# Optimization experiments

Hardware: AMD Instinct MI355X
Metric: run time of the kernel (lower is better)

Reference implementation:

```python
import jax, jax.numpy as jnp
import numpy as np

EPS = 1e-5
CHUNK = 512


def _bn(x, gamma, beta):
    # BatchNorm1d in training mode: biased batch statistics over the batch dim
    m = x.mean(axis=0)
    v = ((x - m) ** 2).mean(axis=0)
    return (x - m) * jax.lax.rsqrt(v + EPS) * gamma + beta


def _xavier(k, fan_in, fan_out):
    lim = float(np.sqrt(6.0 / (fan_in + fan_out)))
    return jax.random.uniform(k, (fan_in, fan_out), minval=-lim, maxval=lim, dtype=jnp.float32)


def setup_inputs() -> dict:
    key = jax.random.key(0)
    ks = jax.random.split(key, 10)
    B, CH_S, CH_H, T = 8192, 512, 2048, 3
    D = CH_H * T  # 6144 = 12 chunks of 512
    inp = {
        "fs": jax.random.normal(ks[0], (B, CH_S), dtype=jnp.float32),
        "ft0": jax.random.normal(ks[1], (B, CH_H), dtype=jnp.float32),
        "ft1": jax.random.normal(ks[2], (B, CH_H), dtype=jnp.float32),
        "ft2": jax.random.normal(ks[3], (B, CH_H), dtype=jnp.float32),
        # fixed (non-trainable in the original: plain tensor) score key [512, 1]
        "score_key": jax.random.uniform(ks[4], (CHUNK, 1), dtype=jnp.float32),
        # align_t: Linear(D,2048) -> BN -> Linear(2048,2048) -> BN -> Linear(2048,CH_H) -> ReLU
        "W1": _xavier(ks[5], D, 2048), "b1": jnp.zeros((2048,), jnp.float32),
        "g1": jnp.ones((2048,), jnp.float32), "beta1": jnp.zeros((2048,), jnp.float32),
        "W2": _xavier(ks[6], 2048, 2048), "b2": jnp.zeros((2048,), jnp.float32),
        "g2": jnp.ones((2048,), jnp.float32), "beta2": jnp.zeros((2048,), jnp.float32),
        "W3": _xavier(ks[7], 2048, CH_H), "b3": jnp.zeros((CH_H,), jnp.float32),
        # extend: Linear(CH_H, D) -> ReLU
        "We": _xavier(ks[8], CH_H, D), "bE": jnp.zeros((D,), jnp.float32),
    }
    return inp


def reference(fs, ft0, ft1, ft2, score_key, W1, b1, g1, beta1, W2, b2, g2, beta2, W3, b3, We, bE):
    # fs is accepted but unused, mirroring the original forward
    ft_all = jnp.concatenate([ft0, ft1, ft2], axis=1)  # [B, D]
    B, D = ft_all.shape
    n_chunks = D // CHUNK
    chunks = ft_all.reshape(B, n_chunks, CHUNK)  # [B, C, 512]
    # chunked score matmul against key[512,1], softmax over chunks
    score = jax.nn.softmax(jnp.einsum("bck,k->bc", chunks, score_key[:, 0]), axis=1)  # [B, C]
    # per-chunk reweighting: x <- x + x*score  == x*(1+score), one broadcasted multiply
    ft_all = (chunks * (1.0 + score[:, :, None])).reshape(B, D)
    # align_t MLP (BatchNorm in training mode, no activation between first layers)
    h = _bn(ft_all @ W1 + b1, g1, beta1)
    h = _bn(h @ W2 + b2, g2, beta2)
    aligned_t = jax.nn.relu(h @ W3 + b3)
    extend_t = jax.nn.relu(aligned_t @ We + bE)
    return aligned_t, extend_t, ft_all
```

## Files before the change

### kernel.cpp

```cpp
#include <hip/hip_runtime.h>
#include <hip/hip_bf16.h>
#include <cstdint>
#include <cstddef>

using bf16x8 = __attribute__((ext_vector_type(8))) __bf16;
using f32x4  = __attribute__((ext_vector_type(4))) float;

__device__ __forceinline__ unsigned short f2bf(float f) {
  unsigned int u = __float_as_uint(f);
  u += 0x7FFFu + ((u >> 16) & 1u);
  return (unsigned short)(u >> 16);
}

__device__ __forceinline__ void async_cp16(const void* g, void* l) {
  __builtin_amdgcn_global_load_lds(
      (const __attribute__((address_space(1))) unsigned int*)g,
      (__attribute__((address_space(3))) unsigned int*)l, 16, 0, 0);
}

__global__ __launch_bounds__(256) void wconv(const float* __restrict__ W,
                                             unsigned short* __restrict__ Wt,
                                             int K, int N) {
  __shared__ float tile[32][33];
  const int n0 = blockIdx.x * 32;
  const int k0 = blockIdx.y * 32;
  const int tx = threadIdx.x;
  const int ty = threadIdx.y;
  for (int i = 0; i < 32; i += 8)
    tile[ty + i][tx] = W[(size_t)(k0 + ty + i) * N + n0 + tx];
  __syncthreads();
  for (int i = 0; i < 32; i += 8)
    Wt[(size_t)(n0 + ty + i) * K + k0 + tx] = f2bf(tile[tx][ty + i]);
}

__global__ __launch_bounds__(256) void score_kernel(
    const float* __restrict__ ft0, const float* __restrict__ ft1,
    const float* __restrict__ ft2, const float* __restrict__ key,
    float* __restrict__ out_f, unsigned short* __restrict__ out_b) {
  const int row  = blockIdx.x;
  const int t    = threadIdx.x;
  const int lane = t & 63;
  const int w    = t >> 6;
  const int h    = t >> 7;
  __shared__ float wsum[6][4];
  __shared__ float mult[12];

  const float4* k4 = (const float4*)key;
  float4 v[6];
#pragma unroll
  for (int i = 0; i < 6; i++) {
    const int idx4 = t + 256 * i;
    const int e    = idx4 * 4;
    const float* tsrc = (i < 2) ? ft0 : (i < 4) ? ft1 : ft2;
    v[i] = *(const float4*)(tsrc + (size_t)row * 2048 + (e & 2047));
    float4 kv = k4[idx4 & 127];
    float p = v[i].x * kv.x + v[i].y * kv.y + v[i].z * kv.z + v[i].w * kv.w;
#pragma unroll
    for (int o = 32; o > 0; o >>= 1) p += __shfl_down(p, o, 64);
    if (lane == 0) wsum[i][w] = p;
  }
  __syncthreads();
  if (t == 0) {
    float s[12];
    float mx = -1e30f;
    for (int c = 0; c < 12; c++) {
      s[c] = wsum[c >> 1][2 * (c & 1)] + wsum[c >> 1][2 * (c & 1) + 1];
      mx = fmaxf(mx, s[c]);
    }
    float tot = 0.f;
    for (int c = 0; c < 12; c++) { s[c] = expf(s[c] - mx); tot += s[c]; }
    const float inv = 1.0f / tot;
    for (int c = 0; c < 12; c++) mult[c] = 1.0f + s[c] * inv;
  }
  __syncthreads();
#pragma unroll
  for (int i = 0; i < 6; i++) {
    const int idx4 = t + 256 * i;
    const int e    = idx4 * 4;
    const float m  = mult[2 * i + h];
    float4 o;
    o.x = v[i].x * m; o.y = v[i].y * m; o.z = v[i].z * m; o.w = v[i].w * m;
    *(float4*)(out_f + (size_t)row * 6144 + e) = o;
    ushort4 ob;
    ob.x = f2bf(o.x); ob.y = f2bf(o.y); ob.z = f2bf(o.z); ob.w = f2bf(o.w);
    *(ushort4*)(out_b + (size_t)row * 6144 + e) = ob;
  }
}

template <int EPI>
__global__ __launch_bounds__(512, 2) void gemm256(
    const unsigned short* __restrict__ A,
    const unsigned short* __restrict__ Bt,
    const float* __restrict__ bias,
    float* __restrict__ C,
    unsigned short* __restrict__ Cbf,
    int M, int N, int K) {
  __shared__ __align__(16) unsigned short smem[65536];
  const int t    = threadIdx.x;
  const int lane = t & 63;
  const int w    = t >> 6;
  const int wm   = w >> 2;
  const int wn   = w & 3;
  const int frow = lane & 15;
  const int quad = lane >> 4;
  const size_t m0 = (size_t)blockIdx.y * 256;
  const size_t n0 = (size_t)blockIdx.x * 256;

  const bool isB  = w >= 4;
  const int  seg  = (w & 3) * 4096;
  const int  off0 = seg + lane * 16;
  const int  pos0 = off0 ^ (((off0 >> 7) & 7) << 4);
  const int  r0   = pos0 >> 6;
  const int  kb0  = pos0 & 63;
  const unsigned short* gp =
      (isB ? Bt + (n0 + (size_t)r0) * K : A + (m0 + (size_t)r0) * K) + (kb0 >> 1);
  char* lseg = (char*)smem + (isB ? 16384 : 0) + seg;

  const int offA = (wm * 128 + frow) * 64 + quad * 16;
  const int aoff = offA ^ (((offA >> 7) & 7) << 4);
  const int offB = (wn * 64 + frow) * 64 + quad * 16;
  const int boff = 16384 + (offB ^ (((offB >> 7) & 7) << 4));

  f32x4 acc[8][4];
  const f32x4 z = {0.f, 0.f, 0.f, 0.f};
#pragma unroll
  for (int i = 0; i < 8; i++)
#pragma unroll
    for (int j = 0; j < 4; j++) acc[i][j] = z;

  const int nkt = K >> 5;

  auto stage = [&](int slot) {
    char* lb = lseg + slot * 32768;
    async_cp16(gp,                  lb);
    async_cp16(gp + (size_t)16 * K, lb + 1024);
    async_cp16(gp + (size_t)32 * K, lb + 2048);
    async_cp16(gp + (size_t)48 * K, lb + 3072);
    gp += 32;
  };

  auto ldfrag = [&](int slot, bf16x8* fa, bf16x8* fb) {
    const char* base = (const char*)smem + slot * 32768;
#pragma unroll
    for (int mi = 0; mi < 8; ++mi)
      fa[mi] = *(const bf16x8*)(base + aoff + mi * 1024);
#pragma unroll
    for (int ni = 0; ni < 4; ++ni)
      fb[ni] = *(const bf16x8*)(base + boff + ni * 1024);
  };

  auto domfma = [&](const bf16x8* fa, const bf16x8* fb) {
    __builtin_amdgcn_s_setprio(1);
#pragma unroll
    for (int mi = 0; mi < 8; ++mi)
#pragma unroll
      for (int ni = 0; ni < 4; ++ni)
        acc[mi][ni] = __builtin_amdgcn_mfma_f32_16x16x32_bf16(fa[mi], fb[ni], acc[mi][ni], 0, 0, 0);
    __builtin_amdgcn_s_setprio(0);
  };

  bf16x8 fa0[8], fb0[4], fa1[8], fb1[4];

  stage(0); stage(1); stage(2);
  asm volatile("s_waitcnt vmcnt(4)\n\ts_barrier" ::: "memory");
  ldfrag(0, fa0, fb0);

  int kt = 0;
  for (; kt + 4 < nkt; kt += 2) {
    stage((kt + 3) & 3);
    domfma(fa0, fb0);
    ldfrag((kt + 1) & 3, fa1, fb1);
    asm volatile("s_waitcnt vmcnt(4)\n\ts_barrier" ::: "memory");
    stage((kt + 4) & 3);
    domfma(fa1, fb1);
    ldfrag((kt + 2) & 3, fa0, fb0);
    asm volatile("s_waitcnt vmcnt(4)\n\ts_barrier" ::: "memory");
  }
  stage((nkt - 1) & 3);
  domfma(fa0, fb0);
  ldfrag((nkt - 3) & 3, fa1, fb1);
  asm volatile("s_waitcnt vmcnt(4)\n\ts_barrier" ::: "memory");
  domfma(fa1, fb1);
  ldfrag((nkt - 2) & 3, fa0, fb0);
  asm volatile("s_waitcnt vmcnt(0)\n\ts_barrier" ::: "memory");
  domfma(fa0, fb0);
  ldfrag((nkt - 1) & 3, fa1, fb1);
  domfma(fa1, fb1);

#pragma unroll
  for (int mi = 0; mi < 8; ++mi) {
    const size_t rowb = m0 + wm * 128 + mi * 16 + quad * 4;
#pragma unroll
    for (int ni = 0; ni < 4; ++ni) {
      const size_t col = n0 + wn * 64 + ni * 16 + frow;
      const float bvs = bias[col];
#pragma unroll
      for (int r = 0; r < 4; ++r) {
        float v = acc[mi][ni][r] + bvs;
        if (EPI == 1) v = fmaxf(v, 0.f);
        const size_t idx = (rowb + r) * (size_t)N + col;
        C[idx] = v;
        if (EPI == 1 && Cbf != nullptr) Cbf[idx] = f2bf(v);
      }
    }
  }
}

__global__ __launch_bounds__(256) void bn_accum(const float* __restrict__ h,
                                                float* __restrict__ ps,
                                                float* __restrict__ pq, int N) {
  const int c  = blockIdx.x * 256 + threadIdx.x;
  const int r0 = blockIdx.y * 256;
  const float* p = h + (size_t)r0 * N + c;
  float s = 0.f, q = 0.f;
  for (int r = 0; r < 256; r++) {
    float x = p[(size_t)r * N];
    s += x; q += x * x;
  }
  ps[(size_t)blockIdx.y * N + c] = s;
  pq[(size_t)blockIdx.y * N + c] = q;
}

__global__ __launch_bounds__(256) void bn_final(const float* __restrict__ ps,
                                                const float* __restrict__ pq,
                                                const float* __restrict__ g,
                                                const float* __restrict__ beta,
                                                float* __restrict__ stats,
                                                int N, int nb, float invM) {
  const int c = blockIdx.x * 256 + threadIdx.x;
  float s = 0.f, q = 0.f;
  for (int b = 0; b < nb; b++) { s += ps[(size_t)b * N + c]; q += pq[(size_t)b * N + c]; }
  const float mean = s * invM;
  const float var  = q * invM - mean * mean;
  const float sc   = g[c] * rsqrtf(var + 1e-5f);
  stats[c]     = sc;
  stats[N + c] = beta[c] - mean * sc;
}

__global__ __launch_bounds__(256) void bn_norm(const float* __restrict__ h,
                                               const float* __restrict__ stats,
                                               unsigned short* __restrict__ hb, int N) {
  const size_t i4 = (size_t)blockIdx.x * 256 + threadIdx.x;
  const float4 x = ((const float4*)h)[i4];
  const int c = (int)((i4 * 4) & (size_t)(N - 1));
  const float4 sc = *(const float4*)(stats + c);
  const float4 tt = *(const float4*)(stats + N + c);
  ushort4 ob;
  ob.x = f2bf(x.x * sc.x + tt.x);
  ob.y = f2bf(x.y * sc.y + tt.y);
  ob.z = f2bf(x.z * sc.z + tt.z);
  ob.w = f2bf(x.w * sc.w + tt.w);
  ((ushort4*)hb)[i4] = ob;
}

extern "C" void kernel_launch(void* const* d_in, const int* in_sizes, int n_in,
                              void* d_out, int out_size, void* d_ws, size_t ws_size,
                              hipStream_t stream) {
  const float* ft0 = (const float*)d_in[1];
  const float* ft1 = (const float*)d_in[2];
  const float* ft2 = (const float*)d_in[3];
  const float* key = (const float*)d_in[4];
  const float* W1  = (const float*)d_in[5];
  const float* b1  = (const float*)d_in[6];
  const float* g1  = (const float*)d_in[7];
  const float* be1 = (const float*)d_in[8];
  const float* W2  = (const float*)d_in[9];
  const float* b2  = (const float*)d_in[10];
  const float* g2  = (const float*)d_in[11];
  const float* be2 = (const float*)d_in[12];
  const float* W3  = (const float*)d_in[13];
  const float* b3  = (const float*)d_in[14];
  const float* We  = (const float*)d_in[15];
  const float* bE  = (const float*)d_in[16];

  float* out         = (float*)d_out;
  float* out_aligned = out;
  float* out_extend  = out + (size_t)8192 * 2048;
  float* out_ft      = out + (size_t)8192 * 2048 + (size_t)8192 * 6144;

  char* ws = (char*)d_ws;
  unsigned short* ft_bf = (unsigned short*)(ws);
  unsigned short* Wt1   = (unsigned short*)(ws + 100663296ull);
  unsigned short* Wt2   = (unsigned short*)(ws + 125829120ull);
  unsigned short* Wt3   = (unsigned short*)(ws + 134217728ull);
  unsigned short* WtE   = (unsigned short*)(ws + 142606336ull);
  float*          hf    = (float*)(ws + 167772160ull);
  unsigned short* hba   = (unsigned short*)(ws + 234881024ull);
  unsigned short* hbb   = (unsigned short*)(ws + 268435456ull);
  float*          psum  = (float*)(ws + 301989888ull);
  float*          psq   = (float*)(ws + 302252032ull);
  float*          stats = (float*)(ws + 302514176ull);

  const dim3 blk32(32, 8);
  wconv<<<dim3(2048 / 32, 6144 / 32), blk32, 0, stream>>>(W1, Wt1, 6144, 2048);
  wconv<<<dim3(2048 / 32, 2048 / 32), blk32, 0, stream>>>(W2, Wt2, 2048, 2048);
  wconv<<<dim3(2048 / 32, 2048 / 32), blk32, 0, stream>>>(W3, Wt3, 2048, 2048);
  wconv<<<dim3(6144 / 32, 2048 / 32), blk32, 0, stream>>>(We, WtE, 2048, 6144);

  score_kernel<<<dim3(8192), dim3(256), 0, stream>>>(ft0, ft1, ft2, key, out_ft, ft_bf);

  gemm256<0><<<dim3(8, 32), dim3(512), 0, stream>>>(ft_bf, Wt1, b1, hf,
                                                    (unsigned short*)nullptr, 8192, 2048, 6144);
  bn_accum<<<dim3(8, 32), dim3(256), 0, stream>>>(hf, psum, psq, 2048);
  bn_final<<<dim3(8), dim3(256), 0, stream>>>(psum, psq, g1, be1, stats, 2048, 32, 1.0f / 8192.0f);
  bn_norm<<<dim3(16384), dim3(256), 0, stream>>>(hf, stats, hba, 2048);

  gemm256<0><<<dim3(8, 32), dim3(512), 0, stream>>>(hba, Wt2, b2, hf,
                                                    (unsigned short*)nullptr, 8192, 2048, 2048);
  bn_accum<<<dim3(8, 32), dim3(256), 0, stream>>>(hf, psum, psq, 2048);
  bn_final<<<dim3(8), dim3(256), 0, stream>>>(psum, psq, g2, be2, stats, 2048, 32, 1.0f / 8192.0f);
  bn_norm<<<dim3(16384), dim3(256), 0, stream>>>(hf, stats, hba, 2048);

  gemm256<1><<<dim3(8, 32), dim3(512), 0, stream>>>(hba, Wt3, b3, out_aligned, hbb,
                                                    8192, 2048, 2048);
  gemm256<1><<<dim3(24, 32), dim3(512), 0, stream>>>(hbb, WtE, bE, out_extend,
                                                     (unsigned short*)nullptr, 8192, 6144, 2048);
}
```

Before: 1.333 ms.

## Fuse BatchNorm partial sums into GEMM epilogue and remap blocks across XCDs

The two bn_accum passes are removed. Per-column sum and sum-of-squares are now computed inside the GEMM epilogue using wave shuffles and a small shared-memory reduction, so each 256-row tile writes its partials directly. This avoids re-reading the 64MB fp32 activation twice. The block index is also remapped so that neighbouring tiles land on the same XCD, which should improve L2 reuse of the A and B panels. In exchange the epilogue gets extra registers, a barrier and more LDS, and the remap assumes the grid dimensions divide evenly by 2 and 4.

```diff
diff --git a/kernel.cpp b/kernel.cpp
--- a/kernel.cpp
+++ b/kernel.cpp
@@ -94,8 +94,11 @@
     const float* __restrict__ bias,
     float* __restrict__ C,
     unsigned short* __restrict__ Cbf,
+    float* __restrict__ ps,
+    float* __restrict__ pq,
     int M, int N, int K) {
   __shared__ __align__(16) unsigned short smem[65536];
+  __shared__ float bnred[8][4][16][2];
   const int t    = threadIdx.x;
   const int lane = t & 63;
   const int w    = t >> 6;
@@ -103,8 +106,17 @@
   const int wn   = w & 3;
   const int frow = lane & 15;
   const int quad = lane >> 4;
-  const size_t m0 = (size_t)blockIdx.y * 256;
-  const size_t n0 = (size_t)blockIdx.x * 256;
+
+  const int NXg  = gridDim.x, NYg = gridDim.y;
+  const int blin = blockIdx.x + NXg * blockIdx.y;
+  const int rxcd = blin & 7;
+  const int ib   = blin >> 3;
+  const int RX   = NXg >> 1;
+  const int RY   = NYg >> 2;
+  const int bx   = (rxcd & 1) * RX + ib % RX;
+  const int by   = (rxcd >> 1) * RY + ib / RX;
+  const size_t m0 = (size_t)by * 256;
+  const size_t n0 = (size_t)bx * 256;
 
   const bool isB  = w >= 4;
   const int  seg  = (w & 3) * 4096;
@@ -187,6 +199,8 @@
   ldfrag((nkt - 1) & 3, fa1, fb1);
   domfma(fa1, fb1);
 
+  float s4[4] = {0.f, 0.f, 0.f, 0.f};
+  float q4[4] = {0.f, 0.f, 0.f, 0.f};
 #pragma unroll
   for (int mi = 0; mi < 8; ++mi) {
     const size_t rowb = m0 + wm * 128 + mi * 16 + quad * 4;
@@ -201,24 +215,37 @@
         const size_t idx = (rowb + r) * (size_t)N + col;
         C[idx] = v;
         if (EPI == 1 && Cbf != nullptr) Cbf[idx] = f2bf(v);
+        if (EPI == 0) { s4[ni] += v; q4[ni] += v * v; }
       }
     }
   }
-}
-
-__global__ __launch_bounds__(256) void bn_accum(const float* __restrict__ h,
-                                                float* __restrict__ ps,
-                                                float* __restrict__ pq, int N) {
-  const int c  = blockIdx.x * 256 + threadIdx.x;
-  const int r0 = blockIdx.y * 256;
-  const float* p = h + (size_t)r0 * N + c;
-  float s = 0.f, q = 0.f;
-  for (int r = 0; r < 256; r++) {
-    float x = p[(size_t)r * N];
-    s += x; q += x * x;
-  }
-  ps[(size_t)blockIdx.y * N + c] = s;
-  pq[(size_t)blockIdx.y * N + c] = q;
+  if (EPI == 0) {
+#pragma unroll
+    for (int ni = 0; ni < 4; ++ni) {
+      s4[ni] += __shfl_down(s4[ni], 16, 64);
+      s4[ni] += __shfl_down(s4[ni], 32, 64);
+      q4[ni] += __shfl_down(q4[ni], 16, 64);
+      q4[ni] += __shfl_down(q4[ni], 32, 64);
+    }
+    if (quad == 0) {
+#pragma unroll
+      for (int ni = 0; ni < 4; ++ni) {
+        bnred[w][ni][frow][0] = s4[ni];
+        bnred[w][ni][frow][1] = q4[ni];
+      }
+    }
+    __syncthreads();
+    if (w < 4 && quad == 0) {
+#pragma unroll
+      for (int ni = 0; ni < 4; ++ni) {
+        const size_t col = n0 + (size_t)w * 64 + ni * 16 + frow;
+        const float ss = bnred[w][ni][frow][0] + bnred[w + 4][ni][frow][0];
+        const float qq = bnred[w][ni][frow][1] + bnred[w + 4][ni][frow][1];
+        ps[(size_t)by * N + col] = ss;
+        pq[(size_t)by * N + col] = qq;
+      }
+    }
+  }
 }
 
 __global__ __launch_bounds__(256) void bn_final(const float* __restrict__ ps,
@@ -300,19 +327,22 @@
   score_kernel<<<dim3(8192), dim3(256), 0, stream>>>(ft0, ft1, ft2, key, out_ft, ft_bf);
 
   gemm256<0><<<dim3(8, 32), dim3(512), 0, stream>>>(ft_bf, Wt1, b1, hf,
-                                                    (unsigned short*)nullptr, 8192, 2048, 6144);
-  bn_accum<<<dim3(8, 32), dim3(256), 0, stream>>>(hf, psum, psq, 2048);
+                                                    (unsigned short*)nullptr, psum, psq,
+                                                    8192, 2048, 6144);
   bn_final<<<dim3(8), dim3(256), 0, stream>>>(psum, psq, g1, be1, stats, 2048, 32, 1.0f / 8192.0f);
   bn_norm<<<dim3(16384), dim3(256), 0, stream>>>(hf, stats, hba, 2048);
 
   gemm256<0><<<dim3(8, 32), dim3(512), 0, stream>>>(hba, Wt2, b2, hf,
-                                                    (unsigned short*)nullptr, 8192, 2048, 2048);
-  bn_accum<<<dim3(8, 32), dim3(256), 0, stream>>>(hf, psum, psq, 2048);
+                                                    (unsigned short*)nullptr, psum, psq,
+                                                    8192, 2048, 2048);
   bn_final<<<dim3(8), dim3(256), 0, stream>>>(psum, psq, g2, be2, stats, 2048, 32, 1.0f / 8192.0f);
   bn_norm<<<dim3(16384), dim3(256), 0, stream>>>(hf, stats, hba, 2048);
 
   gemm256<1><<<dim3(8, 32), dim3(512), 0, stream>>>(hba, Wt3, b3, out_aligned, hbb,
+                                                    (float*)nullptr, (float*)nullptr,
                                                     8192, 2048, 2048);
   gemm256<1><<<dim3(24, 32), dim3(512), 0, stream>>>(hbb, WtE, bE, out_extend,
-                                                     (unsigned short*)nullptr, 8192, 6144, 2048);
-}
+                                                     (unsigned short*)nullptr,
+                                                     (float*)nullptr, (float*)nullptr,
+                                                     8192, 6144, 2048);
+}
```

Result: no change. 1.345 ms (+0.9%).
